# Performance work log

Hardware: AMD Instinct MI355X
Metric: run time of the kernel (lower is better)

Reference implementation:

```python
import jax, jax.numpy as jnp
import numpy as np

NB_NEIGHBORS = 16
RADIUS = 0.25
SPLIT = 32
FEATURE_SIZE = 128
FEATS = (256, 128, 32)
N = 50000


def setup_inputs() -> dict:
    key = jax.random.key(0)
    ks = jax.random.split(key, 12)
    def lin(k, fan_in, fan_out):
        bound = 1.0 / np.sqrt(fan_in)
        kw, kb = jax.random.split(k)
        W = jax.random.uniform(kw, (fan_in, fan_out), jnp.float32, -bound, bound)
        b = jax.random.uniform(kb, (fan_out,), jnp.float32, -bound, bound)
        return W, b
    points = jax.random.normal(ks[0], (N, 3), jnp.float32)
    features = jax.random.normal(ks[1], (N, SPLIT + FEATURE_SIZE), jnp.float32)
    batch = jnp.sort(jax.random.randint(ks[2], (N,), 0, 32, jnp.int64))
    # neighborhood decoder modeled as linear: split -> nb_neighbors*3
    W_nbh, b_nbh = lin(ks[3], SPLIT, NB_NEIGHBORS * 3)
    W1, b1 = lin(ks[4], FEATURE_SIZE + 3, FEATS[0])
    W2, b2 = lin(ks[5], FEATS[0], FEATS[1])
    W3, b3 = lin(ks[6], FEATS[1], FEATS[2])
    return {"points": points, "features": features, "batch": batch,
            "W_nbh": W_nbh, "b_nbh": b_nbh,
            "W1": W1, "b1": b1, "W2": W2, "b2": b2, "W3": W3, "b3": b3}


def reference(points, features, batch, W_nbh, b_nbh, W1, b1, W2, b2, W3, b3):
    point_features = features[:, :SPLIT]            # [N, split]
    feature_features = features[:, SPLIT:]          # [N, feature_size]
    # neighborhood decoder: per-point relative offsets for nb_neighbors points
    relative_points = (point_features @ W_nbh + b_nbh).reshape(-1, 3)  # [N*nb, 3]
    output_batch = jnp.repeat(batch, NB_NEIGHBORS)                     # [N*nb]
    features_repeated = jnp.repeat(feature_features, NB_NEIGHBORS, axis=0)  # [N*nb, fs]
    concat = jnp.concatenate([relative_points, features_repeated], axis=1)  # [N*nb, fs+3]
    h = jax.nn.relu(concat @ W1 + b1)
    h = jax.nn.relu(h @ W2 + b2)
    fc3_features = jax.nn.relu(h @ W3 + b3)
    anchor_points = jnp.repeat(points, NB_NEIGHBORS, axis=0)  # [N*nb, 3]
    output_points = anchor_points + relative_points * RADIUS
    return (output_points, fc3_features, output_batch)
```

## Files before the change

kernel.cpp:

```cpp
#include <hip/hip_runtime.h>


#define NPTS 50000
#define MROWS (NPTS * 16)
#define OFF_FC3 ((size_t)MROWS * 3)
#define OFF_BATCH ((size_t)MROWS * 35)

typedef unsigned int uint_;
typedef unsigned short ushort_;
typedef __attribute__((ext_vector_type(8))) short bf16x8s;
typedef __attribute__((ext_vector_type(16))) float f32x16;

#define MFMA(a, b, c) __builtin_amdgcn_mfma_f32_32x32x16_bf16(a, b, c, 0, 0, 0)
#define CROW(r, h) (((r) & 3) + 8 * ((r) >> 2) + 4 * (h))

#define WS_W2T 0
#define WS_W3T 32768
#define WS_W1PT 36864
#define WS_WNT 69632
#define WS_S 71680
#define WS_REL_BYTES 25743360

__device__ __forceinline__ float bl(uint_ u) { return __uint_as_float(u << 16); }
__device__ __forceinline__ float bh(uint_ u) { return __uint_as_float(u & 0xffff0000u); }
__device__ __forceinline__ ushort_ f2b(float f) {
  uint_ u = __float_as_uint(f);
  u += 0x7fffu + ((u >> 16) & 1u);
  return (ushort_)(u >> 16);
}
__device__ __forceinline__ uint_ cvtpk(float lo, float hi) {
  uint_ r;
  asm("v_cvt_pk_bf16_f32 %0, %1, %2" : "=v"(r) : "v"(lo), "v"(hi));
  return r;
}
__device__ __forceinline__ float relu_(float x) { return fmaxf(x, 0.f); }

template<bool F32>
__device__ __forceinline__ float ldv(const void* p, int i) {
  if (F32) return ((const float*)p)[i];
  return bl((uint_)((const ushort_*)p)[i]);
}

struct F8 { float v[8]; };
template<bool F32>
__device__ __forceinline__ F8 ld8(const void* p, int idx) {
  F8 r;
  if (F32) {
    float4 a = *(const float4*)((const float*)p + idx);
    float4 b = *(const float4*)((const float*)p + idx + 4);
    r.v[0] = a.x; r.v[1] = a.y; r.v[2] = a.z; r.v[3] = a.w;
    r.v[4] = b.x; r.v[5] = b.y; r.v[6] = b.z; r.v[7] = b.w;
  } else {
    uint4 u = *(const uint4*)((const ushort_*)p + idx);
    r.v[0] = bl(u.x); r.v[1] = bh(u.x); r.v[2] = bl(u.y); r.v[3] = bh(u.y);
    r.v[4] = bl(u.z); r.v[5] = bh(u.z); r.v[6] = bl(u.w); r.v[7] = bh(u.w);
  }
  return r;
}

union FragU { uint_ u[4]; uint4 q; bf16x8s v; };
__device__ __forceinline__ bf16x8s pack8(const F8& f) {
  FragU o;
  #pragma unroll
  for (int j = 0; j < 4; ++j) o.u[j] = cvtpk(f.v[2 * j], f.v[2 * j + 1]);
  return o.v;
}

__device__ __forceinline__ bool sniff_f32(const void* feats) {
  const ushort_* u = (const ushort_*)feats;
  int pass = 0;
  #pragma unroll 8
  for (int m = 0; m < 32; ++m) {
    int ex = (u[m] >> 7) & 0xff;
    pass += (ex >= 100 && ex <= 140) ? 1 : 0;
  }
  return pass < 28;
}

__global__ void __launch_bounds__(256)
kT(const void* features, const void* batch, const void* W1, const void* Wn,
   const void* W2, const void* W3, ushort_* wsu, float* out) {
  bool f32 = sniff_f32(features);
  const uint_* bu = (const uint_*)batch;
  int nz = 0;
  #pragma unroll
  for (int m = 0; m < 16; ++m) nz += (bu[49999 - 2 * m] != 0u) ? 1 : 0;
  bool i64 = (nz == 0);

  const int total = 32768 + 32768 + 4096 + 2048 + 800000;
  for (int i = blockIdx.x * 256 + threadIdx.x; i < total; i += gridDim.x * 256) {
    if (i < 32768) {
      int n = i & 255, k = i >> 8;
      wsu[WS_W1PT + n * 128 + k] = f32 ? f2b(((const float*)W1)[(3 + k) * 256 + n])
                                       : ((const ushort_*)W1)[(3 + k) * 256 + n];
    } else if (i < 65536) {
      int i2 = i - 32768, n = i2 & 127, k = i2 >> 7;
      wsu[WS_W2T + n * 256 + k] = f32 ? f2b(((const float*)W2)[k * 128 + n])
                                      : ((const ushort_*)W2)[k * 128 + n];
    } else if (i < 69632) {
      int i3 = i - 65536, n = i3 & 31, k = i3 >> 5;
      wsu[WS_W3T + n * 128 + k] = f32 ? f2b(((const float*)W3)[k * 32 + n])
                                      : ((const ushort_*)W3)[k * 32 + n];
    } else if (i < 71680) {
      int i4 = i - 69632, n = i4 >> 5, k = i4 & 31;
      ushort_ v = 0;
      if (n < 48) v = f32 ? f2b(((const float*)Wn)[k * 48 + n])
                          : ((const ushort_*)Wn)[k * 48 + n];
      wsu[WS_WNT + n * 32 + k] = v;
    } else {
      int g = i - 71680;
      int idx = g >> 4;
      int v = i64 ? (int)bu[2 * idx] : ((const int*)batch)[idx];
      out[OFF_BATCH + (size_t)g] = (float)v;
    }
  }
}

template<bool F32>
__device__ void runS(const void* points, const void* features, const void* bn,
                     const void* b1, ushort_* wsu, float* out,
                     ushort_* w1pt, ushort_* feats) {
  const ushort_* W1pT_ws = wsu + WS_W1PT;
  const ushort_* WnT_ws = wsu + WS_WNT;
  ushort_* S_ws = wsu + WS_S;
  float* rel_ws = (float*)((char*)wsu + WS_REL_BYTES);
  const int tid = threadIdx.x;

  for (int c = tid; c < 4096; c += 256) {
    int n = c >> 4, s = c & 15;
    uint4 src = *(const uint4*)(W1pT_ws + c * 8);
    *(uint4*)((char*)w1pt + n * 256 + ((s * 16) ^ ((n & 7) << 4))) = src;
  }

  const int w = tid >> 6, lane = tid & 63, l31 = lane & 31, h = lane >> 5, h8 = h * 8;
  const int mt = w & 1, ctb = (w >> 1) * 4, ctr = w >> 1;

  for (int tile = blockIdx.x; tile < 782; tile += gridDim.x) {
    const int pbase = tile * 64;
    for (int c = tid; c < 2048; c += 256) {
      int row = c >> 5, c4 = c & 31;
      int p = pbase + row;
      uint2 d = {0u, 0u};
      if (p < NPTS) {
        if (F32) {
          float4 v = *(const float4*)((const float*)features + p * 160 + 32 + c4 * 4);
          d.x = cvtpk(v.x, v.y); d.y = cvtpk(v.z, v.w);
        } else {
          d = *(const uint2*)((const ushort_*)features + p * 160 + 32 + c4 * 4);
        }
      }
      *(uint2*)((char*)feats + row * 256 + ((c4 * 8) ^ ((row & 7) << 4))) = d;
    }
    __syncthreads();

    bf16x8s af[8];
    #pragma unroll
    for (int ks = 0; ks < 8; ++ks) {
      int row = mt * 32 + l31;
      af[ks] = *(const bf16x8s*)((const char*)feats + row * 256 +
                                 (((ks * 16 + h8) * 2) ^ ((row & 7) << 4)));
    }
    #pragma unroll
    for (int ci = 0; ci < 4; ++ci) {
      int ct = ctb + ci;
      float b1v = ldv<F32>(b1, ct * 32 + l31);
      f32x16 acc;
      #pragma unroll
      for (int r = 0; r < 16; ++r) acc[r] = b1v;
      #pragma unroll
      for (int ks = 0; ks < 8; ++ks) {
        int n = ct * 32 + l31;
        bf16x8s bf = *(const bf16x8s*)((const char*)w1pt + n * 256 +
                                       (((ks * 16 + h8) * 2) ^ ((n & 7) << 4)));
        acc = MFMA(af[ks], bf, acc);
      }
      #pragma unroll
      for (int r = 0; r < 16; ++r) {
        int p = pbase + mt * 32 + CROW(r, h);
        if (p < NPTS)
          S_ws[(p >> 2) * 1024 + (ct * 32 + l31) * 4 + (p & 3)] = f2b(acc[r]);
      }
    }

    {
      int pm = pbase + mt * 32 + l31;
      pm = pm < NPTS ? pm : NPTS - 1;
      bf16x8s ar[2];
      #pragma unroll
      for (int ks = 0; ks < 2; ++ks) {
        F8 v = ld8<F32>(features, pm * 160 + ks * 16 + h8);
        ar[ks] = pack8(v);
      }
      f32x16 acc;
      #pragma unroll
      for (int r = 0; r < 16; ++r) acc[r] = 0.f;
      #pragma unroll
      for (int ks = 0; ks < 2; ++ks) {
        int n = ctr * 32 + l31;
        FragU bw;
        bw.q = *(const uint4*)(WnT_ws + n * 32 + ks * 16 + h8);
        acc = MFMA(ar[ks], bw.v, acc);
      }
      int j = ctr * 32 + l31;
      if (j < 48) {
        float bnv = ldv<F32>(bn, j);
        int c = j - (j / 3) * 3;
        #pragma unroll
        for (int r = 0; r < 16; ++r) {
          int p = pbase + mt * 32 + CROW(r, h);
          if (p < NPTS) {
            float rv = acc[r] + bnv;
            rel_ws[p * 48 + j] = rv;
            out[(size_t)p * 48 + j] = ldv<F32>(points, p * 3 + c) + 0.25f * rv;
          }
        }
      }
    }
    __syncthreads();
  }
}

__global__ void __launch_bounds__(256, 2)
kS(const void* points, const void* features, const void* bn, const void* b1,
   ushort_* wsu, float* out) {
  __shared__ ushort_ w1pt[32768];
  __shared__ ushort_ feats[8192];
  if (sniff_f32(features))
    runS<true>(points, features, bn, b1, wsu, out, w1pt, feats);
  else
    runS<false>(points, features, bn, b1, wsu, out, w1pt, feats);
}

__device__ __forceinline__ bf16x8s assemble(const f32x16& a, int base) {
  uint_ A0 = cvtpk(relu_(a[base + 0]), relu_(a[base + 1]));
  uint_ A1 = cvtpk(relu_(a[base + 2]), relu_(a[base + 3]));
  uint_ B0 = cvtpk(relu_(a[base + 4]), relu_(a[base + 5]));
  uint_ B1 = cvtpk(relu_(a[base + 6]), relu_(a[base + 7]));
  asm("v_permlane32_swap_b32 %0, %1" : "+v"(A0), "+v"(B0));
  asm("v_permlane32_swap_b32 %0, %1" : "+v"(A1), "+v"(B1));
  FragU o;
  o.u[0] = A0;
  o.u[1] = A1;
  o.u[2] = B0;
  o.u[3] = B1;
  return o.v;
}

template<bool F32>
__device__ void runM(const void* W1, const void* b2, const void* b3,
                     const ushort_* wsu, float* out,
                     ushort_* w2t, ushort_* w3t, uint_* w1x, float* b2f, float* b3f) {
  const ushort_* S4 = wsu + WS_S;
  const float* rel_ws = (const float*)((const char*)wsu + WS_REL_BYTES);
  const int tid = threadIdx.x;

  for (int c = tid; c < 4608; c += 512) {
    if (c < 4096) {
      int n = c >> 5, s = c & 31;
      uint4 src = *(const uint4*)(wsu + WS_W2T + c * 8);
      *(uint4*)((char*)w2t + n * 512 + ((s * 16) ^ ((n & 7) << 4))) = src;
    } else {
      int c2 = c - 4096, n = c2 >> 4, s = c2 & 15;
      uint4 src = *(const uint4*)(wsu + WS_W3T + c2 * 8);
      *(uint4*)((char*)w3t + n * 256 + ((s * 16) ^ ((n & 7) << 4))) = src;
    }
  }
  if (tid < 256) {
    float w0 = ldv<F32>(W1, 0 * 256 + tid);
    float w1v = ldv<F32>(W1, 1 * 256 + tid);
    float w2v = ldv<F32>(W1, 2 * 256 + tid);
    w1x[tid * 2 + 0] = cvtpk(w0, w1v);
    w1x[tid * 2 + 1] = cvtpk(w2v, 0.f);
  }
  if (tid < 128) b2f[tid] = ldv<F32>(b2, tid);
  if (tid < 32) b3f[tid] = ldv<F32>(b3, tid);
  __syncthreads();

  const int w = tid >> 6, lane = tid & 63, l31 = lane & 31, h = lane >> 5;
  const int slot = blockIdx.x * 8 + w;
  const int stride = gridDim.x * 8;

  f32x16 zero16;
  #pragma unroll
  for (int r = 0; r < 16; ++r) zero16[r] = 0.f;

  FragU yone;
  yone.u[0] = h ? 0u : cvtpk(1.0f, 0.f);
  yone.u[1] = 0u; yone.u[2] = 0u; yone.u[3] = 0u;
  FragU xb[4];
  #pragma unroll
  for (int mt = 0; mt < 4; ++mt) {
    xb[mt].u[0] = h ? 0u : cvtpk(b2f[mt * 32 + l31], 0.f);
    xb[mt].u[1] = 0u; xb[mt].u[2] = 0u; xb[mt].u[3] = 0u;
  }
  float4 b3v[4];
  #pragma unroll
  for (int q = 0; q < 4; ++q) b3v[q] = *(const float4*)(b3f + q * 8 + 4 * h);

  for (int g = slot; g < 12500; g += stride) {
    const int p0 = g * 4;

    bf16x8s yf[2];
    #pragma unroll
    for (int t = 0; t < 2; ++t) {
      int p = p0 + 2 * t + (l31 >> 4);
      const float* rp = rel_ws + p * 48 + (l31 & 15) * 3;
      float r0 = rp[0], r1 = rp[1], r2 = rp[2];
      float selA = (l31 >> 4) ? 0.f : 1.f;
      float selB = 1.f - selA;
      FragU y;
      y.u[0] = h ? 0u : cvtpk(r0, r1);
      y.u[1] = h ? 0u : cvtpk(r2, selA);
      y.u[2] = h ? 0u : cvtpk(selB, 0.f);
      y.u[3] = 0u;
      yf[t] = y.v;
    }

    f32x16 accA[4], accB[4];
    #pragma unroll
    for (int mt = 0; mt < 4; ++mt) {
      accA[mt] = MFMA(xb[mt].v, yone.v, zero16);
      accB[mt] = MFMA(xb[mt].v, yone.v, zero16);
    }

    #pragma unroll
    for (int grp = 0; grp < 8; ++grp) {
      const int c0 = grp * 32;
      uint2 sq = *(const uint2*)(S4 + (size_t)g * 1024 + (c0 + l31) * 4);
      uint2 wp = *(const uint2*)(w1x + (c0 + l31) * 2);
      FragU x0, x1;
      x0.u[0] = h ? 0u : wp.x;
      x0.u[1] = h ? 0u : (wp.y | (sq.x << 16));
      x0.u[2] = h ? 0u : (sq.x >> 16);
      x0.u[3] = 0u;
      x1.u[0] = h ? 0u : wp.x;
      x1.u[1] = h ? 0u : (wp.y | (sq.y << 16));
      x1.u[2] = h ? 0u : (sq.y >> 16);
      x1.u[3] = 0u;
      f32x16 acc10 = MFMA(x0.v, yf[0], zero16);
      f32x16 acc11 = MFMA(x1.v, yf[1], zero16);
      #pragma unroll
      for (int b = 0; b < 2; ++b) {
        bf16x8s hA = assemble(acc10, b * 8);
        bf16x8s hB = assemble(acc11, b * 8);
        const int kb = (c0 + b * 16 + h * 8) * 2;
        #pragma unroll
        for (int mt = 0; mt < 4; ++mt) {
          int n = mt * 32 + l31;
          bf16x8s af = *(const bf16x8s*)((const char*)w2t + n * 512 +
                                         (kb ^ ((n & 7) << 4)));
          accA[mt] = MFMA(af, hA, accA[mt]);
          accB[mt] = MFMA(af, hB, accB[mt]);
        }
      }
    }

    f32x16 o3A, o3B;
    #pragma unroll
    for (int ks3 = 0; ks3 < 8; ++ks3) {
      int kb = (ks3 * 16 + h * 8) * 2;
      bf16x8s a3 = *(const bf16x8s*)((const char*)w3t + l31 * 256 +
                                     (kb ^ ((l31 & 7) << 4)));
      const int mt = ks3 >> 1, base = (ks3 & 1) * 8;
      bf16x8s B3A = assemble(accA[mt], base);
      bf16x8s B3B = assemble(accB[mt], base);
      if (ks3 == 0) {
        o3A = MFMA(a3, B3A, zero16);
        o3B = MFMA(a3, B3B, zero16);
      } else {
        o3A = MFMA(a3, B3A, o3A);
        o3B = MFMA(a3, B3B, o3B);
      }
    }

    const size_t rowA = (size_t)p0 * 16 + l31;
    #pragma unroll
    for (int q = 0; q < 4; ++q) {
      float4 vA = {relu_(o3A[4 * q] + b3v[q].x), relu_(o3A[4 * q + 1] + b3v[q].y),
                   relu_(o3A[4 * q + 2] + b3v[q].z), relu_(o3A[4 * q + 3] + b3v[q].w)};
      float4 vB = {relu_(o3B[4 * q] + b3v[q].x), relu_(o3B[4 * q + 1] + b3v[q].y),
                   relu_(o3B[4 * q + 2] + b3v[q].z), relu_(o3B[4 * q + 3] + b3v[q].w)};
      *(float4*)(out + OFF_FC3 + rowA * 32 + q * 8 + 4 * h) = vA;
      *(float4*)(out + OFF_FC3 + (rowA + 32) * 32 + q * 8 + 4 * h) = vB;
    }
  }
}

__global__ void __launch_bounds__(512, 2)
kM(const void* features, const void* W1, const void* b2, const void* b3,
   const ushort_* wsu, float* out) {
  __shared__ ushort_ w2t[32768];
  __shared__ ushort_ w3t[4096];
  __shared__ uint_ w1x[512];
  __shared__ float b2f[128];
  __shared__ float b3f[32];
  if (sniff_f32(features))
    runM<true>(W1, b2, b3, wsu, out, w2t, w3t, w1x, b2f, b3f);
  else
    runM<false>(W1, b2, b3, wsu, out, w2t, w3t, w1x, b2f, b3f);
}

extern "C" void kernel_launch(void* const* d_in, const int* in_sizes, int n_in,
                              void* d_out, int out_size, void* d_ws, size_t ws_size,
                              hipStream_t stream) {
  const void* points   = d_in[0];
  const void* features = d_in[1];
  const void* batch    = d_in[2];
  const void* Wn = d_in[3];  const void* bn = d_in[4];
  const void* W1 = d_in[5];  const void* b1 = d_in[6];
  const void* W2 = d_in[7];  const void* b2 = d_in[8];
  const void* W3 = d_in[9];  const void* b3 = d_in[10];
  float* out = (float*)d_out;
  ushort_* wsu = (ushort_*)d_ws;

  hipLaunchKernelGGL(kT, dim3(512), dim3(256), 0, stream,
                     features, batch, W1, Wn, W2, W3, wsu, out);
  hipLaunchKernelGGL(kS, dim3(782), dim3(256), 0, stream,
                     points, features, bn, b1, wsu, out);
  hipLaunchKernelGGL(kM, dim3(512), dim3(512), 0, stream,
                     features, W1, b2, b3, wsu, out);
}
```

Before: 134.9 us.

## Move batch output into MLP kernel, vectorize S stores, prefetch S, read W3 from global

The batch-to-float output is moved from the weight-transpose kernel into the main MLP kernel, so kT only transposes weights and uses a smaller grid. The per-element bf16 S stores in kS become packed uint2 stores, and kM prefetches all eight S fragments at the top of each group. W3 is read straight from workspace instead of being staged in LDS, and the W2 MFMA block runs under raised wave priority. kM's grid goes from 512 to 782 blocks; with two 512-thread blocks per CU that may mean an uneven tail wave.

```diff
diff --git a/kernel.cpp b/kernel.cpp
--- a/kernel.cpp
+++ b/kernel.cpp
@@ -78,41 +78,28 @@
 }
 
 __global__ void __launch_bounds__(256)
-kT(const void* features, const void* batch, const void* W1, const void* Wn,
-   const void* W2, const void* W3, ushort_* wsu, float* out) {
+kT(const void* features, const void* W1, const void* Wn,
+   const void* W2, const void* W3, ushort_* wsu) {
   bool f32 = sniff_f32(features);
-  const uint_* bu = (const uint_*)batch;
-  int nz = 0;
-  #pragma unroll
-  for (int m = 0; m < 16; ++m) nz += (bu[49999 - 2 * m] != 0u) ? 1 : 0;
-  bool i64 = (nz == 0);
-
-  const int total = 32768 + 32768 + 4096 + 2048 + 800000;
-  for (int i = blockIdx.x * 256 + threadIdx.x; i < total; i += gridDim.x * 256) {
-    if (i < 32768) {
-      int n = i & 255, k = i >> 8;
-      wsu[WS_W1PT + n * 128 + k] = f32 ? f2b(((const float*)W1)[(3 + k) * 256 + n])
-                                       : ((const ushort_*)W1)[(3 + k) * 256 + n];
-    } else if (i < 65536) {
-      int i2 = i - 32768, n = i2 & 127, k = i2 >> 7;
-      wsu[WS_W2T + n * 256 + k] = f32 ? f2b(((const float*)W2)[k * 128 + n])
-                                      : ((const ushort_*)W2)[k * 128 + n];
-    } else if (i < 69632) {
-      int i3 = i - 65536, n = i3 & 31, k = i3 >> 5;
-      wsu[WS_W3T + n * 128 + k] = f32 ? f2b(((const float*)W3)[k * 32 + n])
-                                      : ((const ushort_*)W3)[k * 32 + n];
-    } else if (i < 71680) {
-      int i4 = i - 69632, n = i4 >> 5, k = i4 & 31;
-      ushort_ v = 0;
-      if (n < 48) v = f32 ? f2b(((const float*)Wn)[k * 48 + n])
-                          : ((const ushort_*)Wn)[k * 48 + n];
-      wsu[WS_WNT + n * 32 + k] = v;
-    } else {
-      int g = i - 71680;
-      int idx = g >> 4;
-      int v = i64 ? (int)bu[2 * idx] : ((const int*)batch)[idx];
-      out[OFF_BATCH + (size_t)g] = (float)v;
-    }
+  int i = blockIdx.x * 256 + threadIdx.x;
+  if (i < 32768) {
+    int n = i & 255, k = i >> 8;
+    wsu[WS_W1PT + n * 128 + k] = f32 ? f2b(((const float*)W1)[(3 + k) * 256 + n])
+                                     : ((const ushort_*)W1)[(3 + k) * 256 + n];
+  } else if (i < 65536) {
+    int i2 = i - 32768, n = i2 & 127, k = i2 >> 7;
+    wsu[WS_W2T + n * 256 + k] = f32 ? f2b(((const float*)W2)[k * 128 + n])
+                                    : ((const ushort_*)W2)[k * 128 + n];
+  } else if (i < 69632) {
+    int i3 = i - 65536, n = i3 & 31, k = i3 >> 5;
+    wsu[WS_W3T + n * 128 + k] = f32 ? f2b(((const float*)W3)[k * 32 + n])
+                                    : ((const ushort_*)W3)[k * 32 + n];
+  } else {
+    int i4 = i - 69632, n = i4 >> 5, k = i4 & 31;
+    ushort_ v = 0;
+    if (n < 48) v = f32 ? f2b(((const float*)Wn)[k * 48 + n])
+                        : ((const ushort_*)Wn)[k * 48 + n];
+    wsu[WS_WNT + n * 32 + k] = v;
   }
 }
 
@@ -175,10 +162,14 @@
         acc = MFMA(af[ks], bf, acc);
       }
       #pragma unroll
-      for (int r = 0; r < 16; ++r) {
-        int p = pbase + mt * 32 + CROW(r, h);
-        if (p < NPTS)
-          S_ws[(p >> 2) * 1024 + (ct * 32 + l31) * 4 + (p & 3)] = f2b(acc[r]);
+      for (int q = 0; q < 4; ++q) {
+        int prow = pbase + mt * 32 + 8 * q + 4 * h;
+        if (prow < NPTS) {
+          uint2 d2;
+          d2.x = cvtpk(acc[4 * q + 0], acc[4 * q + 1]);
+          d2.y = cvtpk(acc[4 * q + 2], acc[4 * q + 3]);
+          *(uint2*)(S_ws + (prow >> 2) * 1024 + (ct * 32 + l31) * 4) = d2;
+        }
       }
     }
 
@@ -247,23 +238,18 @@
 }
 
 template<bool F32>
-__device__ void runM(const void* W1, const void* b2, const void* b3,
-                     const ushort_* wsu, float* out,
-                     ushort_* w2t, ushort_* w3t, uint_* w1x, float* b2f, float* b3f) {
+__device__ void runM(const void* batch, const void* W1, const void* b2,
+                     const void* b3, const ushort_* wsu, float* out,
+                     ushort_* w2t, uint_* w1x, float* b2f, float* b3f, int* ib64) {
   const ushort_* S4 = wsu + WS_S;
+  const ushort_* W3T = wsu + WS_W3T;
   const float* rel_ws = (const float*)((const char*)wsu + WS_REL_BYTES);
   const int tid = threadIdx.x;
 
-  for (int c = tid; c < 4608; c += 512) {
-    if (c < 4096) {
-      int n = c >> 5, s = c & 31;
-      uint4 src = *(const uint4*)(wsu + WS_W2T + c * 8);
-      *(uint4*)((char*)w2t + n * 512 + ((s * 16) ^ ((n & 7) << 4))) = src;
-    } else {
-      int c2 = c - 4096, n = c2 >> 4, s = c2 & 15;
-      uint4 src = *(const uint4*)(wsu + WS_W3T + c2 * 8);
-      *(uint4*)((char*)w3t + n * 256 + ((s * 16) ^ ((n & 7) << 4))) = src;
-    }
+  for (int c = tid; c < 4096; c += 512) {
+    int n = c >> 5, s = c & 31;
+    uint4 src = *(const uint4*)(wsu + WS_W2T + c * 8);
+    *(uint4*)((char*)w2t + n * 512 + ((s * 16) ^ ((n & 7) << 4))) = src;
   }
   if (tid < 256) {
     float w0 = ldv<F32>(W1, 0 * 256 + tid);
@@ -274,7 +260,15 @@
   }
   if (tid < 128) b2f[tid] = ldv<F32>(b2, tid);
   if (tid < 32) b3f[tid] = ldv<F32>(b3, tid);
+  if (tid == 0) {
+    const uint_* bu = (const uint_*)batch;
+    int nz = 0;
+    #pragma unroll
+    for (int m = 0; m < 16; ++m) nz += (bu[49999 - 2 * m] != 0u) ? 1 : 0;
+    ib64[0] = (nz == 0) ? 1 : 0;
+  }
   __syncthreads();
+  const int i64f = ib64[0];
 
   const int w = tid >> 6, lane = tid & 63, l31 = lane & 31, h = lane >> 5;
   const int slot = blockIdx.x * 8 + w;
@@ -299,6 +293,13 @@
 
   for (int g = slot; g < 12500; g += stride) {
     const int p0 = g * 4;
+
+    uint2 sq[8];
+    #pragma unroll
+    for (int grp = 0; grp < 8; ++grp)
+      sq[grp] = *(const uint2*)(S4 + (size_t)g * 1024 + (grp * 32 + l31) * 4);
+    int pb = p0 + (lane >> 4);
+    int bv = i64f ? (int)((const uint_*)batch)[2 * pb] : ((const int*)batch)[pb];
 
     bf16x8s yf[2];
     #pragma unroll
@@ -316,6 +317,8 @@
       yf[t] = y.v;
     }
 
+    out[OFF_BATCH + (size_t)g * 64 + lane] = (float)bv;
+
     f32x16 accA[4], accB[4];
     #pragma unroll
     for (int mt = 0; mt < 4; ++mt) {
@@ -326,16 +329,16 @@
     #pragma unroll
     for (int grp = 0; grp < 8; ++grp) {
       const int c0 = grp * 32;
-      uint2 sq = *(const uint2*)(S4 + (size_t)g * 1024 + (c0 + l31) * 4);
+      uint2 sg = sq[grp];
       uint2 wp = *(const uint2*)(w1x + (c0 + l31) * 2);
       FragU x0, x1;
       x0.u[0] = h ? 0u : wp.x;
-      x0.u[1] = h ? 0u : (wp.y | (sq.x << 16));
-      x0.u[2] = h ? 0u : (sq.x >> 16);
+      x0.u[1] = h ? 0u : (wp.y | (sg.x << 16));
+      x0.u[2] = h ? 0u : (sg.x >> 16);
       x0.u[3] = 0u;
       x1.u[0] = h ? 0u : wp.x;
-      x1.u[1] = h ? 0u : (wp.y | (sq.y << 16));
-      x1.u[2] = h ? 0u : (sq.y >> 16);
+      x1.u[1] = h ? 0u : (wp.y | (sg.y << 16));
+      x1.u[2] = h ? 0u : (sg.y >> 16);
       x1.u[3] = 0u;
       f32x16 acc10 = MFMA(x0.v, yf[0], zero16);
       f32x16 acc11 = MFMA(x1.v, yf[1], zero16);
@@ -344,6 +347,7 @@
         bf16x8s hA = assemble(acc10, b * 8);
         bf16x8s hB = assemble(acc11, b * 8);
         const int kb = (c0 + b * 16 + h * 8) * 2;
+        __builtin_amdgcn_s_setprio(1);
         #pragma unroll
         for (int mt = 0; mt < 4; ++mt) {
           int n = mt * 32 + l31;
@@ -352,15 +356,14 @@
           accA[mt] = MFMA(af, hA, accA[mt]);
           accB[mt] = MFMA(af, hB, accB[mt]);
         }
+        __builtin_amdgcn_s_setprio(0);
       }
     }
 
     f32x16 o3A, o3B;
     #pragma unroll
     for (int ks3 = 0; ks3 < 8; ++ks3) {
-      int kb = (ks3 * 16 + h * 8) * 2;
-      bf16x8s a3 = *(const bf16x8s*)((const char*)w3t + l31 * 256 +
-                                     (kb ^ ((l31 & 7) << 4)));
+      bf16x8s a3 = *(const bf16x8s*)(W3T + l31 * 128 + ks3 * 16 + h * 8);
       const int mt = ks3 >> 1, base = (ks3 & 1) * 8;
       bf16x8s B3A = assemble(accA[mt], base);
       bf16x8s B3B = assemble(accB[mt], base);
@@ -387,17 +390,17 @@
 }
 
 __global__ void __launch_bounds__(512, 2)
-kM(const void* features, const void* W1, const void* b2, const void* b3,
-   const ushort_* wsu, float* out) {
+kM(const void* features, const void* batch, const void* W1, const void* b2,
+   const void* b3, const ushort_* wsu, float* out) {
   __shared__ ushort_ w2t[32768];
-  __shared__ ushort_ w3t[4096];
   __shared__ uint_ w1x[512];
   __shared__ float b2f[128];
   __shared__ float b3f[32];
+  __shared__ int ib64[1];
   if (sniff_f32(features))
-    runM<true>(W1, b2, b3, wsu, out, w2t, w3t, w1x, b2f, b3f);
+    runM<true>(batch, W1, b2, b3, wsu, out, w2t, w1x, b2f, b3f, ib64);
   else
-    runM<false>(W1, b2, b3, wsu, out, w2t, w3t, w1x, b2f, b3f);
+    runM<false>(batch, W1, b2, b3, wsu, out, w2t, w1x, b2f, b3f, ib64);
 }
 
 extern "C" void kernel_launch(void* const* d_in, const int* in_sizes, int n_in,
@@ -413,10 +416,10 @@
   float* out = (float*)d_out;
   ushort_* wsu = (ushort_*)d_ws;
 
-  hipLaunchKernelGGL(kT, dim3(512), dim3(256), 0, stream,
-                     features, batch, W1, Wn, W2, W3, wsu, out);
+  hipLaunchKernelGGL(kT, dim3(280), dim3(256), 0, stream,
+                     features, W1, Wn, W2, W3, wsu);
   hipLaunchKernelGGL(kS, dim3(782), dim3(256), 0, stream,
                      points, features, bn, b1, wsu, out);
-  hipLaunchKernelGGL(kM, dim3(512), dim3(512), 0, stream,
-                     features, W1, b2, b3, wsu, out);
-}
+  hipLaunchKernelGGL(kM, dim3(782), dim3(512), 0, stream,
+                     features, batch, W1, b2, b3, wsu, out);
+}
```

After: 141.8 us. 5.2% more time.
